# Optimization experiments

Hardware: AMD Instinct MI355X
Metric: run time of the kernel (lower is better)

The kernel has to match this reference:

```python
import jax, jax.numpy as jnp
import numpy as np

B, N_NODES, T_IN = 512, 32, 12
HID, HEADS, OUT_CH, DEG = 64, 8, 9, 8


def setup_inputs() -> dict:
    key = jax.random.key(0)
    ks = jax.random.split(key, 26)
    rn = lambda k, s, sc=0.1: (jax.random.normal(k, s, jnp.float32) * sc)
    E = B * N_NODES * DEG
    src = jax.random.randint(ks[0], (E,), 0, N_NODES, jnp.int32)
    dst = jax.random.randint(ks[1], (E,), 0, N_NODES, jnp.int32)
    off = jnp.repeat(jnp.arange(B, dtype=jnp.int32) * N_NODES, N_NODES * DEG)
    edge_index = jnp.stack([src + off, dst + off])  # block-diagonal batched graph
    x = jax.random.normal(ks[2], (B, N_NODES, T_IN), jnp.float32)
    return {
        "x": x,
        "edge_index": edge_index,
        # gat1: in=T_IN -> HEADS*HID, concat
        "W1": rn(ks[3], (T_IN, HEADS * HID)),
        "a_src1": rn(ks[4], (HEADS, HID)),
        "a_dst1": rn(ks[5], (HEADS, HID)),
        "b1": rn(ks[6], (HEADS * HID,), 0.01),
        # gat2: in=HEADS*HID -> HID, heads=1, mean (concat=False)
        "W2": rn(ks[7], (HEADS * HID, HID), 0.05),
        "a_src2": rn(ks[8], (1, HID)),
        "a_dst2": rn(ks[9], (1, HID)),
        "b2": rn(ks[10], (HID,), 0.01),
        "gamma": jnp.ones((HID,), jnp.float32),
        "beta": jnp.zeros((HID,), jnp.float32),
        # gru1: input_size=N_NODES(=32), hidden=HID
        "Wi1": rn(ks[11], (3 * HID, N_NODES)),
        "Wh1": rn(ks[12], (3 * HID, HID)),
        "bi1": rn(ks[13], (3 * HID,), 0.01),
        "bh1": rn(ks[14], (3 * HID,), 0.01),
        # gru2: input_size=HID, hidden=HID
        "Wi2": rn(ks[15], (3 * HID, HID)),
        "Wh2": rn(ks[16], (3 * HID, HID)),
        "bi2": rn(ks[17], (3 * HID,), 0.01),
        "bh2": rn(ks[18], (3 * HID,), 0.01),
        "Wf": rn(ks[19], (OUT_CH, HID)),
        "bf": rn(ks[20], (OUT_CH,), 0.01),
    }


def _gat_layer(x, src, dst, W, a_s, a_d, b, concat):
    # PyG GATConv (eval mode, self-loops already appended by caller)
    Nn = x.shape[0]
    heads, hc = a_s.shape
    h = (x @ W).reshape(Nn, heads, hc)                 # [N, H, C]
    es = jnp.sum(h * a_s, axis=-1)                     # [N, H]
    ed = jnp.sum(h * a_d, axis=-1)
    e = jax.nn.leaky_relu(es[src] + ed[dst], 0.2)      # [E, H]
    m = jax.ops.segment_max(e, dst, num_segments=Nn)
    p = jnp.exp(e - m[dst])
    s = jax.ops.segment_sum(p, dst, num_segments=Nn)
    alpha = p / (s[dst] + 1e-16)                       # per-dst softmax
    out = jax.ops.segment_sum(h[src] * alpha[:, :, None], dst, num_segments=Nn)
    out = out.reshape(Nn, heads * hc) if concat else out.mean(axis=1)
    return out + b


def _gru(x, Wi, Wh, bi, bh):
    # torch.nn.GRU (batch_first) single layer; x: [B, T, F]
    H = Wh.shape[1]
    xi = x @ Wi.T + bi                                 # [B, T, 3H]
    def step(h, xt):
        gh = h @ Wh.T + bh
        r = jax.nn.sigmoid(xt[:, :H] + gh[:, :H])
        z = jax.nn.sigmoid(xt[:, H:2 * H] + gh[:, H:2 * H])
        n = jnp.tanh(xt[:, 2 * H:] + r * gh[:, 2 * H:])
        hn = (1.0 - z) * n + z * h
        return hn, hn
    h0 = jnp.zeros((x.shape[0], H), x.dtype)
    _, ys = jax.lax.scan(step, h0, jnp.swapaxes(xi, 0, 1))
    return jnp.swapaxes(ys, 0, 1)


def reference(x, edge_index, W1, a_src1, a_dst1, b1, W2, a_src2, a_dst2, b2,
              gamma, beta, Wi1, Wh1, bi1, bh1, Wi2, Wh2, bi2, bh2, Wf, bf):
    Bsz, Nn_, T = x.shape
    Nn = Bsz * Nn_
    xf = x.reshape(Nn, T)                              # dropout is identity in eval
    sl = jnp.arange(Nn, dtype=edge_index.dtype)        # PyG add_self_loops=True
    src = jnp.concatenate([edge_index[0], sl])
    dst = jnp.concatenate([edge_index[1], sl])
    h = jax.nn.elu(_gat_layer(xf, src, dst, W1, a_src1, a_dst1, b1, True))
    h = jax.nn.elu(_gat_layer(h, src, dst, W2, a_src2, a_dst2, b2, False))
    mu = h.mean(-1, keepdims=True)
    var = ((h - mu) ** 2).mean(-1, keepdims=True)
    h = (h - mu) / jnp.sqrt(var + 1e-5) * gamma + beta
    seq = h.reshape(Bsz, Nn_, -1).transpose(0, 2, 1)   # [B, HID(seq), N_NODES(feat)]
    g = _gru(seq, Wi1, Wh1, bi1, bh1)
    g = _gru(g, Wi2, Wh2, bi2, bh2)
    return g[:, -1, :] @ Wf.T + bf                     # [B, OUT_CH]
```

## Files before the change

### kernel.cpp

```cpp
#include <hip/hip_runtime.h>
#include <hip/hip_bf16.h>
#include <stdint.h>

#define BATCH 512
#define NN 32
#define T_IN 12
#define HID 64
#define HEADS 8
#define OUT_CH 9
#define EPB (NN*8)
#define ETOT (EPB+NN)
#define F1 (HEADS*HID)

using u16 = unsigned short;
using u32 = unsigned int;
typedef _Float16 f16;
typedef _Float16 f16x2 __attribute__((ext_vector_type(2)));

__device__ __forceinline__ float bf2f(u16 u){ return __uint_as_float(((u32)u)<<16); }
__device__ __forceinline__ u16 f2bf(float f){
    u32 x = __float_as_uint(f);
    u32 r = (x + 0x7FFFu + ((x>>16)&1u))>>16;
    return (u16)r;
}
__device__ __forceinline__ u32 packf16(float a, float b){
    f16x2 p; p.x=(f16)a; p.y=(f16)b; return __builtin_bit_cast(u32,p);
}
__device__ __forceinline__ u16 f2h16(float a){ f16 h=(f16)a; return __builtin_bit_cast(u16,h); }
__device__ __forceinline__ float lof(u32 w){ return (float)__builtin_bit_cast(f16x2,w).x; }
__device__ __forceinline__ float hif(u32 w){ return (float)__builtin_bit_cast(f16x2,w).y; }
__device__ __forceinline__ float dot2(u32 a, u32 b, float c){
#if __has_builtin(__builtin_amdgcn_fdot2)
    return __builtin_amdgcn_fdot2(__builtin_bit_cast(f16x2,a), __builtin_bit_cast(f16x2,b), c, false);
#else
    return fmaf(lof(a),lof(b), fmaf(hif(a),hif(b), c));
#endif
}
__device__ __forceinline__ float elu1(float x){ return x > 0.f ? x : (__expf(x)-1.f); }
__device__ __forceinline__ float sigm(float x){ return 1.f/(1.f+__expf(-x)); }
__device__ __forceinline__ float tanh_(float x){ return 1.f - 2.f/(__expf(2.f*x)+1.f); }

__global__ __launch_bounds__(256) void k_detect(const u32* __restrict__ xw, int* __restrict__ flag){
    __shared__ int cnt;
    if(threadIdx.x==0) cnt=0;
    __syncthreads();
    int c=0;
    for(int i=threadIdx.x;i<4096;i+=256){
        u32 w=xw[i];
        if(w & 0x7FFFFFFFu){
            u32 el=(w>>7)&0xFFu;
            if(el>=0x90u) c++;
        }
    }
    atomicAdd(&cnt,c);
    __syncthreads();
    if(threadIdx.x==0) *flag = (cnt>256) ? 1 : 0;
}

struct CvtDesc {
    const void* src[20];
    void*       dst[20];
    int         n[20];
};

__global__ __launch_bounds__(256) void k_convert(CvtDesc d, const int* __restrict__ flag){
    const int seg = blockIdx.x;
    const int f = *flag;
    const void* s = d.src[seg];
    const int n = d.n[seg];
    const int stride = gridDim.y*256;
    float* o=(float*)d.dst[seg];
    for(int i=blockIdx.y*256+threadIdx.x;i<n;i+=stride)
        o[i] = f ? ((const float*)s)[i] : bf2f(((const u16*)s)[i]);
}

__global__ __launch_bounds__(256) void k_w2i(const void* __restrict__ W2src, u16* __restrict__ W2i,
                                             const int* __restrict__ flag){
    int i = blockIdx.x*256+threadIdx.x;
    int k=i>>6, j=i&63;
    float v = (*flag)? ((const float*)W2src)[i] : bf2f(((const u16*)W2src)[i]);
    W2i[ (((size_t)(k>>3)*64 + j)<<3) + (k&7) ] = f2h16(v);
}

__global__ __launch_bounds__(256,2) void k_gat1(
    const float* __restrict__ x, const int* __restrict__ ei,
    const float* __restrict__ W1, const float* __restrict__ a_s, const float* __restrict__ a_d,
    const float* __restrict__ b1, u32* __restrict__ h1g)
{
    const int b = blockIdx.x, t = threadIdx.x;
    __shared__ __align__(16) float s_x[NN][12];
    __shared__ float s_W1[T_IN*F1];
    __shared__ __align__(16) u16 s_h[NN][520];
    __shared__ u32 s_aspk[HEADS*32], s_adpk[HEADS*32];
    __shared__ float s_es[NN][HEADS], s_ed[NN][HEADS];
    __shared__ unsigned char s_src[ETOT], s_dst[ETOT];
    __shared__ float s_al[ETOT][HEADS];
    __shared__ int s_cnt[NN], s_off[NN], s_fil[NN];
    __shared__ short s_lst[ETOT];

    for(int i=t;i<NN*T_IN;i+=256) s_x[i/12][i%12] = x[b*NN*T_IN + i];
    for(int i=t;i<T_IN*F1;i+=256) s_W1[i]=W1[i];
    s_aspk[t]=packf16(a_s[2*t],a_s[2*t+1]);
    s_adpk[t]=packf16(a_d[2*t],a_d[2*t+1]);
    if(t<EPB){
        s_src[t] = (unsigned char)(ei[b*EPB+t] - b*NN);
        s_dst[t] = (unsigned char)(ei[(size_t)BATCH*EPB + b*EPB+t] - b*NN);
    }
    if(t<NN){ s_src[EPB+t]=s_dst[EPB+t]=(unsigned char)t; s_cnt[t]=0; s_fil[t]=0; }
    __syncthreads();

    {
        float w0[12], w1[12];
        #pragma unroll
        for(int k=0;k<12;k++){ w0[k]=s_W1[k*F1+t]; w1[k]=s_W1[k*F1+t+256]; }
        for(int n=0;n<NN;n++){
            float xr[12];
            const float4* xp=(const float4*)s_x[n];
            *(float4*)&xr[0]=xp[0]; *(float4*)&xr[4]=xp[1]; *(float4*)&xr[8]=xp[2];
            float A=0.f,B=0.f;
            #pragma unroll
            for(int k=0;k<12;k++){ A=fmaf(xr[k],w0[k],A); B=fmaf(xr[k],w1[k],B); }
            s_h[n][t]=f2h16(A); s_h[n][t+256]=f2h16(B);
        }
    }
    for(int e=t;e<ETOT;e+=256) atomicAdd(&s_cnt[s_dst[e]],1);
    __syncthreads();

    {
        int n=t&31, hd=t>>5;
        const uint4* hp=(const uint4*)((const u16*)s_h[n] + hd*64);
        u32 hw[32];
        #pragma unroll
        for(int q=0;q<8;q++) *(uint4*)&hw[q*4]=hp[q];
        float e1=0.f,e2=0.f;
        #pragma unroll
        for(int k=0;k<32;k++){ e1=dot2(hw[k],s_aspk[hd*32+k],e1); e2=dot2(hw[k],s_adpk[hd*32+k],e2); }
        s_es[n][hd]=e1; s_ed[n][hd]=e2;
    }
    if(t==0){ int o=0; for(int i=0;i<NN;i++){ s_off[i]=o; o+=s_cnt[i]; } }
    __syncthreads();

    for(int e=t;e<ETOT;e+=256){
        int d=s_dst[e]; int p=atomicAdd(&s_fil[d],1); s_lst[s_off[d]+p]=(short)e;
    }
    for(int e=t;e<ETOT;e+=256){
        int s=s_src[e], d=s_dst[e];
        #pragma unroll
        for(int hd=0;hd<HEADS;hd++){
            float v = s_es[s][hd]+s_ed[d][hd];
            s_al[e][hd] = v>0.f? v : 0.2f*v;
        }
    }
    __syncthreads();

    {
        int d=t>>3, hd=t&7;
        int o=s_off[d], c=s_cnt[d];
        float m=-1e30f;
        for(int i=0;i<c;i++) m = fmaxf(m, s_al[s_lst[o+i]][hd]);
        float ss=0.f;
        for(int i=0;i<c;i++){ int e=s_lst[o+i]; float p=__expf(s_al[e][hd]-m); s_al[e][hd]=p; ss+=p; }
        float inv = 1.f/(ss+1e-16f);
        for(int i=0;i<c;i++) s_al[s_lst[o+i]][hd]*=inv;
    }
    __syncthreads();

    {
        int d=t&31, hd=t>>5;
        int o=s_off[d], cnt=s_cnt[d];
        size_t obase = ((size_t)(b*NN+d))*256 + hd*32;
        #pragma unroll
        for(int ch=0;ch<4;ch++){
            float acc[16];
            #pragma unroll
            for(int i=0;i<16;i++) acc[i]=0.f;
            for(int i=0;i<cnt;i++){
                int e=s_lst[o+i]; float a=s_al[e][hd]; int sr=s_src[e];
                const uint4* hp=(const uint4*)((const u16*)s_h[sr] + hd*64 + ch*16);
                u32 pw[8];
                *(uint4*)&pw[0]=hp[0]; *(uint4*)&pw[4]=hp[1];
                #pragma unroll
                for(int q=0;q<8;q++){ acc[2*q]+=a*lof(pw[q]); acc[2*q+1]+=a*hif(pw[q]); }
            }
            u32* op = h1g + obase + ch*8;
            #pragma unroll
            for(int j=0;j<8;j++){
                float v0=elu1(acc[2*j]   + b1[hd*64+ch*16+2*j]);
                float v1=elu1(acc[2*j+1] + b1[hd*64+ch*16+2*j+1]);
                op[j]=packf16(v0,v1);
            }
        }
    }
}

__global__ __launch_bounds__(256,2) void k_gat2ln(
    const u32* __restrict__ h1g, const int* __restrict__ ei,
    const uint4* __restrict__ W2i, const float* __restrict__ a_s2, const float* __restrict__ a_d2,
    const float* __restrict__ b2, const float* __restrict__ gam, const float* __restrict__ bet,
    float* __restrict__ hlng)
{
    const int b=blockIdx.x, t=threadIdx.x;
    __shared__ __align__(16) u32 s_h1[NN*260];
    __shared__ float s_h2[NN][HID];
    __shared__ float s_es[NN], s_ed[NN];
    __shared__ unsigned char s_src[ETOT], s_dst[ETOT];
    __shared__ float s_al[ETOT];
    __shared__ int s_cnt[NN], s_off[NN], s_fil[NN];
    __shared__ short s_lst[ETOT];

    { const u32* g = h1g + (size_t)b*8192;
      for(int w=t; w<8192; w+=256){ int n=w>>8, c=w&255; s_h1[n*260+c]=g[w]; } }
    if(t<EPB){
        s_src[t]=(unsigned char)(ei[b*EPB+t]-b*NN);
        s_dst[t]=(unsigned char)(ei[(size_t)BATCH*EPB+b*EPB+t]-b*NN);
    }
    if(t<NN){ s_src[EPB+t]=s_dst[EPB+t]=(unsigned char)t; s_cnt[t]=0; s_fil[t]=0; }
    __syncthreads();

    for(int e=t;e<ETOT;e+=256) atomicAdd(&s_cnt[s_dst[e]],1);
    {
        int n0=(t>>4)<<1, j0=(t&15)<<2;
        const u32* r0=&s_h1[n0*260];
        const u32* r1=&s_h1[(n0+1)*260];
        float a00=0,a01=0,a02=0,a03=0,a10=0,a11=0,a12=0,a13=0;
        for(int kb=0;kb<64;kb++){
            uint4 A0=*(const uint4*)&r0[kb*4];
            uint4 A1=*(const uint4*)&r1[kb*4];
            const uint4* wp=&W2i[kb*64+j0];
            uint4 w0=wp[0], w1=wp[1], w2=wp[2], w3=wp[3];
            a00=dot2(A0.x,w0.x,a00); a00=dot2(A0.y,w0.y,a00); a00=dot2(A0.z,w0.z,a00); a00=dot2(A0.w,w0.w,a00);
            a01=dot2(A0.x,w1.x,a01); a01=dot2(A0.y,w1.y,a01); a01=dot2(A0.z,w1.z,a01); a01=dot2(A0.w,w1.w,a01);
            a02=dot2(A0.x,w2.x,a02); a02=dot2(A0.y,w2.y,a02); a02=dot2(A0.z,w2.z,a02); a02=dot2(A0.w,w2.w,a02);
            a03=dot2(A0.x,w3.x,a03); a03=dot2(A0.y,w3.y,a03); a03=dot2(A0.z,w3.z,a03); a03=dot2(A0.w,w3.w,a03);
            a10=dot2(A1.x,w0.x,a10); a10=dot2(A1.y,w0.y,a10); a10=dot2(A1.z,w0.z,a10); a10=dot2(A1.w,w0.w,a10);
            a11=dot2(A1.x,w1.x,a11); a11=dot2(A1.y,w1.y,a11); a11=dot2(A1.z,w1.z,a11); a11=dot2(A1.w,w1.w,a11);
            a12=dot2(A1.x,w2.x,a12); a12=dot2(A1.y,w2.y,a12); a12=dot2(A1.z,w2.z,a12); a12=dot2(A1.w,w2.w,a12);
            a13=dot2(A1.x,w3.x,a13); a13=dot2(A1.y,w3.y,a13); a13=dot2(A1.z,w3.z,a13); a13=dot2(A1.w,w3.w,a13);
        }
        s_h2[n0][j0]=a00; s_h2[n0][j0+1]=a01; s_h2[n0][j0+2]=a02; s_h2[n0][j0+3]=a03;
        s_h2[n0+1][j0]=a10; s_h2[n0+1][j0+1]=a11; s_h2[n0+1][j0+2]=a12; s_h2[n0+1][j0+3]=a13;
    }
    __syncthreads();

    {
        int n=t>>3, g=t&7;
        float e1=0,e2=0;
        #pragma unroll
        for(int cc=0; cc<8; cc++){
            float hv = s_h2[n][g*8+cc];
            e1 += hv*a_s2[g*8+cc];
            e2 += hv*a_d2[g*8+cc];
        }
        #pragma unroll
        for(int m=1;m<8;m<<=1){ e1 += __shfl_xor(e1,m,64); e2 += __shfl_xor(e2,m,64); }
        if(g==0){ s_es[n]=e1; s_ed[n]=e2; }
    }
    if(t==0){ int o=0; for(int i=0;i<NN;i++){ s_off[i]=o; o+=s_cnt[i]; } }
    __syncthreads();

    for(int e=t;e<ETOT;e+=256){
        int d=s_dst[e]; int p=atomicAdd(&s_fil[d],1); s_lst[s_off[d]+p]=(short)e;
    }
    for(int e=t;e<ETOT;e+=256){
        float v = s_es[s_src[e]] + s_ed[s_dst[e]];
        s_al[e] = v>0.f? v:0.2f*v;
    }
    __syncthreads();

    if(t<NN){
        int o=s_off[t], c=s_cnt[t];
        float m=-1e30f;
        for(int i=0;i<c;i++) m=fmaxf(m, s_al[s_lst[o+i]]);
        float ss=0;
        for(int i=0;i<c;i++){int e=s_lst[o+i]; float p=__expf(s_al[e]-m); s_al[e]=p; ss+=p;}
        float inv=1.f/(ss+1e-16f);
        for(int i=0;i<c;i++) s_al[s_lst[o+i]]*=inv;
    }
    __syncthreads();

    {
        int n=t>>3, g=t&7;
        float acc[8];
        #pragma unroll
        for(int i=0;i<8;i++) acc[i]=0;
        int o=s_off[n], cnt=s_cnt[n];
        for(int i=0;i<cnt;i++){
            int e=s_lst[o+i]; float a=s_al[e]; int sr=s_src[e];
            const float4* hp=(const float4*)&s_h2[sr][g*8];
            float4 v0=hp[0], v1=hp[1];
            acc[0]+=a*v0.x; acc[1]+=a*v0.y; acc[2]+=a*v0.z; acc[3]+=a*v0.w;
            acc[4]+=a*v1.x; acc[5]+=a*v1.y; acc[6]+=a*v1.z; acc[7]+=a*v1.w;
        }
        float sum=0,sq=0;
        #pragma unroll
        for(int i=0;i<8;i++){
            float v = elu1(acc[i] + b2[g*8+i]);
            acc[i]=v; sum+=v; sq+=v*v;
        }
        #pragma unroll
        for(int m=1;m<8;m<<=1){ sum+=__shfl_xor(sum,m,64); sq+=__shfl_xor(sq,m,64); }
        float mu = sum*(1.f/64.f);
        float var = sq*(1.f/64.f) - mu*mu;
        float rs = rsqrtf(var + 1e-5f);
        float* outp = hlng + (size_t)b*HID*NN;
        #pragma unroll
        for(int i=0;i<8;i++){
            int c=g*8+i;
            float v=(acc[i]-mu)*rs*gam[c] + bet[c];
            outp[c*NN + n] = v;
        }
    }
}

__global__ __launch_bounds__(256,2) void k_gruf(
    const float* __restrict__ hlng,
    const float* __restrict__ Wi1, const float* __restrict__ Wh1,
    const float* __restrict__ bi1, const float* __restrict__ bh1,
    const float* __restrict__ Wi2, const float* __restrict__ Wh2,
    const float* __restrict__ bi2, const float* __restrict__ bh2,
    const float* __restrict__ Wf, const float* __restrict__ bfv,
    void* __restrict__ outp, const int* __restrict__ flag)
{
    const int b=blockIdx.x, t=threadIdx.x;
    const int wave=t>>6, lane=t&63;
    const int layer=wave>>1;
    const int s=wave&1;
    const int u=lane;

    __shared__ __align__(16) u32 s_x1[64*16];
    __shared__ __align__(16) u32 s_y[2][32];
    __shared__ __align__(16) u32 s_h1w[32];
    __shared__ __align__(16) u32 s_h2w[32];
    __shared__ float s_p1[4*64];
    __shared__ float s_p2[4*64];
    __shared__ float s_h2f[64];

    { const float2* g=(const float2*)(hlng + (size_t)b*2048);
      for(int w=t;w<1024;w+=256){ float2 v=g[w]; s_x1[w]=packf16(v.x,v.y); } }
    if(t<32){ s_h1w[t]=0u; s_h2w[t]=0u; }

    u32 wiR[16],wiZ[16],wiN[16],whR[16],whZ[16],whN[16];
    if(layer==0){
        const float2* WiF=(const float2*)Wi1;
        const float2* WhF=(const float2*)Wh1;
        #pragma unroll
        for(int k=0;k<8;k++){
            float2 a=WiF[u*16+s*8+k], c=WiF[(64+u)*16+s*8+k], d=WiF[(128+u)*16+s*8+k];
            wiR[k]=packf16(a.x,a.y); wiZ[k]=packf16(c.x,c.y); wiN[k]=packf16(d.x,d.y);
        }
        #pragma unroll
        for(int k=0;k<16;k++){
            float2 a=WhF[u*32+s*16+k], c=WhF[(64+u)*32+s*16+k], d=WhF[(128+u)*32+s*16+k];
            whR[k]=packf16(a.x,a.y); whZ[k]=packf16(c.x,c.y); whN[k]=packf16(d.x,d.y);
        }
    } else {
        const float2* WiF=(const float2*)Wi2;
        const float2* WhF=(const float2*)Wh2;
        #pragma unroll
        for(int k=0;k<16;k++){
            float2 a=WiF[u*32+s*16+k], c=WiF[(64+u)*32+s*16+k], d=WiF[(128+u)*32+s*16+k];
            wiR[k]=packf16(a.x,a.y); wiZ[k]=packf16(c.x,c.y); wiN[k]=packf16(d.x,d.y);
            float2 e=WhF[u*32+s*16+k], f=WhF[(64+u)*32+s*16+k], g2=WhF[(128+u)*32+s*16+k];
            whR[k]=packf16(e.x,e.y); whZ[k]=packf16(f.x,f.y); whN[k]=packf16(g2.x,g2.y);
        }
    }
    float br=0.f,bz=0.f,bxn=0.f,bhn=0.f,h=0.f;
    if(s==0){
        const float* bi = layer? bi2:bi1;
        const float* bh = layer? bh2:bh1;
        br=bi[u]+bh[u]; bz=bi[64+u]+bh[64+u]; bxn=bi[128+u]; bhn=bh[128+u];
    }
    float* sp = layer? s_p2 : s_p1;
    __syncthreads();

    for(int it=0; it<=64; ++it){
        float pr=0.f,pz=0.f,pxn=0.f,phn=0.f;
        bool act;
        if(layer==0){
            act = (it<64);
            if(act){
                u32 xw[8], hw[16];
                const uint4* xp=(const uint4*)&s_x1[it*16+s*8];
                *(uint4*)&xw[0]=xp[0]; *(uint4*)&xw[4]=xp[1];
                const uint4* hp=(const uint4*)&s_h1w[s*16];
                #pragma unroll
                for(int q=0;q<4;q++) *(uint4*)&hw[q*4]=hp[q];
                #pragma unroll
                for(int k=0;k<8;k++){ pr=dot2(xw[k],wiR[k],pr); pz=dot2(xw[k],wiZ[k],pz); pxn=dot2(xw[k],wiN[k],pxn); }
                #pragma unroll
                for(int k=0;k<16;k++){ pr=dot2(hw[k],whR[k],pr); pz=dot2(hw[k],whZ[k],pz); phn=dot2(hw[k],whN[k],phn); }
            }
        } else {
            act = (it>=1);
            if(act){
                u32 xw[16], hw[16];
                const uint4* xp=(const uint4*)&s_y[(it-1)&1][s*16];
                #pragma unroll
                for(int q=0;q<4;q++) *(uint4*)&xw[q*4]=xp[q];
                const uint4* hp=(const uint4*)&s_h2w[s*16];
                #pragma unroll
                for(int q=0;q<4;q++) *(uint4*)&hw[q*4]=hp[q];
                #pragma unroll
                for(int k=0;k<16;k++){
                    pr=dot2(xw[k],wiR[k],pr); pz=dot2(xw[k],wiZ[k],pz); pxn=dot2(xw[k],wiN[k],pxn);
                    pr=dot2(hw[k],whR[k],pr); pz=dot2(hw[k],whZ[k],pz); phn=dot2(hw[k],whN[k],phn);
                }
            }
        }
        if(act && s==1){ sp[u]=pr; sp[64+u]=pz; sp[128+u]=pxn; sp[192+u]=phn; }
        __syncthreads();
        if(act && s==0){
            float ar = pr + sp[u] + br;
            float az = pz + sp[64+u] + bz;
            float axn = pxn + sp[128+u] + bxn;
            float ahn = phn + sp[192+u] + bhn;
            float r=sigm(ar), z=sigm(az);
            float n=tanh_(axn + r*ahn);
            h=(1.f-z)*n + z*h;
            u16 hp16=f2h16(h);
            if(layer==0){
                ((u16*)s_h1w)[u]=hp16;
                ((u16*)s_y[it&1])[u]=hp16;
            } else {
                ((u16*)s_h2w)[u]=hp16;
                if(it==64) s_h2f[u]=h;
            }
        }
        __syncthreads();
    }

    if(t<OUT_CH){
        float acc=bfv[t];
        #pragma unroll
        for(int i=0;i<64;i++) acc += s_h2f[i]*Wf[t*64+i];
        if(*flag) ((float*)outp)[b*OUT_CH+t]=acc;
        else      ((u16*)outp)[b*OUT_CH+t]=f2bf(acc);
    }
}

extern "C" void kernel_launch(void* const* d_in, const int* in_sizes, int n_in,
                              void* d_out, int out_size, void* d_ws, size_t ws_size,
                              hipStream_t stream)
{
    char* ws=(char*)d_ws;
    int* flag = (int*)ws;
    float* cf = (float*)(ws + 256);
    float* c_x   = cf; cf+=196608;
    float* c_W1  = cf; cf+=6144;
    float* c_as1 = cf; cf+=512;
    float* c_ad1 = cf; cf+=512;
    float* c_b1  = cf; cf+=512;
    float* c_as2 = cf; cf+=64;
    float* c_ad2 = cf; cf+=64;
    float* c_b2  = cf; cf+=64;
    float* c_gam = cf; cf+=64;
    float* c_bet = cf; cf+=64;
    float* c_Wi1 = cf; cf+=6144;
    float* c_Wh1 = cf; cf+=12288;
    float* c_bi1 = cf; cf+=192;
    float* c_bh1 = cf; cf+=192;
    float* c_Wi2 = cf; cf+=12288;
    float* c_Wh2 = cf; cf+=12288;
    float* c_bi2 = cf; cf+=192;
    float* c_bh2 = cf; cf+=192;
    float* c_Wf  = cf; cf+=576;
    float* c_bf  = cf; cf+=9;
    uintptr_t p = ((uintptr_t)cf + 255) & ~(uintptr_t)255;
    u16* c_W2i = (u16*)p;
    p = (p + 32768*2 + 255) & ~(uintptr_t)255;
    u32* h1g = (u32*)p;
    p = (p + (size_t)BATCH*NN*256*4 + 255) & ~(uintptr_t)255;
    float* hlng = (float*)p;

    const int* ei = (const int*)d_in[1];

    CvtDesc d;
    const int srcIdx[20] = {0,2,3,4,5,7,8,9,10,11,12,13,14,15,16,17,18,19,20,21};
    void* dsts[20] = {c_x,c_W1,c_as1,c_ad1,c_b1,c_as2,c_ad2,c_b2,c_gam,c_bet,
                      c_Wi1,c_Wh1,c_bi1,c_bh1,c_Wi2,c_Wh2,c_bi2,c_bh2,c_Wf,c_bf};
    const int ns[20] = {196608,6144,512,512,512,64,64,64,64,64,
                        6144,12288,192,192,12288,12288,192,192,576,9};
    for(int i=0;i<20;i++){ d.src[i]=d_in[srcIdx[i]]; d.dst[i]=dsts[i]; d.n[i]=ns[i]; }

    k_detect <<<dim3(1),dim3(256),0,stream>>>((const u32*)d_in[0], flag);
    k_convert<<<dim3(20,8),dim3(256),0,stream>>>(d, flag);
    k_w2i    <<<dim3(128),dim3(256),0,stream>>>(d_in[6], c_W2i, flag);
    k_gat1   <<<dim3(BATCH),dim3(256),0,stream>>>(c_x,ei,c_W1,c_as1,c_ad1,c_b1,h1g);
    k_gat2ln <<<dim3(BATCH),dim3(256),0,stream>>>(h1g,ei,(const uint4*)c_W2i,c_as2,c_ad2,c_b2,c_gam,c_bet,hlng);
    k_gruf   <<<dim3(BATCH),dim3(256),0,stream>>>(hlng,c_Wi1,c_Wh1,c_bi1,c_bh1,
                                                  c_Wi2,c_Wh2,c_bi2,c_bh2,c_Wf,c_bf,d_out,flag);
}
```

Before: 262.6 us.

## Parallelize GAT softmax with shared atomics and use wave shuffles in GRU

The per-destination serial softmax loops in both GAT kernels are replaced by edge-parallel passes. These use shared-memory atomicMax on order-preserving encoded floats and atomicAdd for the sums, and normalization is folded into the aggregation epilogue. The GAT1 aggregation now processes 32 channels per pass instead of 16. The GRU kernel splits each hidden unit's dot product across the two half-waves and combines them with a lane shuffle, with double-buffered hidden state. This removes one __syncthreads and the shared-memory partial exchange per timestep, at the cost of atomic contention, more accumulator registers, and a change in floating-point summation order.

```diff
diff --git a/kernel.cpp b/kernel.cpp
--- a/kernel.cpp
+++ b/kernel.cpp
@@ -39,6 +39,13 @@
 __device__ __forceinline__ float elu1(float x){ return x > 0.f ? x : (__expf(x)-1.f); }
 __device__ __forceinline__ float sigm(float x){ return 1.f/(1.f+__expf(-x)); }
 __device__ __forceinline__ float tanh_(float x){ return 1.f - 2.f/(__expf(2.f*x)+1.f); }
+__device__ __forceinline__ u32 fenc(float v){
+    u32 b=__float_as_uint(v);
+    return (b&0x80000000u) ? ~b : (b|0x80000000u);
+}
+__device__ __forceinline__ float fdec(u32 k){
+    return __uint_as_float((k&0x80000000u) ? (k&0x7FFFFFFFu) : ~k);
+}
 
 __global__ __launch_bounds__(256) void k_detect(const u32* __restrict__ xw, int* __restrict__ flag){
     __shared__ int cnt;
@@ -95,6 +102,8 @@
     __shared__ float s_es[NN][HEADS], s_ed[NN][HEADS];
     __shared__ unsigned char s_src[ETOT], s_dst[ETOT];
     __shared__ float s_al[ETOT][HEADS];
+    __shared__ u32 s_mx[NN*HEADS];
+    __shared__ float s_sm[NN*HEADS], s_inv[NN*HEADS];
     __shared__ int s_cnt[NN], s_off[NN], s_fil[NN];
     __shared__ short s_lst[ETOT];
 
@@ -102,6 +111,7 @@
     for(int i=t;i<T_IN*F1;i+=256) s_W1[i]=W1[i];
     s_aspk[t]=packf16(a_s[2*t],a_s[2*t+1]);
     s_adpk[t]=packf16(a_d[2*t],a_d[2*t+1]);
+    s_mx[t]=0u; s_sm[t]=0.f;
     if(t<EPB){
         s_src[t] = (unsigned char)(ei[b*EPB+t] - b*NN);
         s_dst[t] = (unsigned char)(ei[(size_t)BATCH*EPB + b*EPB+t] - b*NN);
@@ -143,50 +153,51 @@
     for(int e=t;e<ETOT;e+=256){
         int d=s_dst[e]; int p=atomicAdd(&s_fil[d],1); s_lst[s_off[d]+p]=(short)e;
     }
-    for(int e=t;e<ETOT;e+=256){
-        int s=s_src[e], d=s_dst[e];
-        #pragma unroll
-        for(int hd=0;hd<HEADS;hd++){
-            float v = s_es[s][hd]+s_ed[d][hd];
-            s_al[e][hd] = v>0.f? v : 0.2f*v;
-        }
-    }
-    __syncthreads();
-
-    {
-        int d=t>>3, hd=t&7;
-        int o=s_off[d], c=s_cnt[d];
-        float m=-1e30f;
-        for(int i=0;i<c;i++) m = fmaxf(m, s_al[s_lst[o+i]][hd]);
-        float ss=0.f;
-        for(int i=0;i<c;i++){ int e=s_lst[o+i]; float p=__expf(s_al[e][hd]-m); s_al[e][hd]=p; ss+=p; }
-        float inv = 1.f/(ss+1e-16f);
-        for(int i=0;i<c;i++) s_al[s_lst[o+i]][hd]*=inv;
-    }
+    for(int i=t;i<ETOT*HEADS;i+=256){
+        int e=i>>3, hd=i&7;
+        int sr=s_src[e], d=s_dst[e];
+        float v = s_es[sr][hd]+s_ed[d][hd];
+        v = v>0.f? v : 0.2f*v;
+        s_al[e][hd]=v;
+        atomicMax(&s_mx[d*8+hd], fenc(v));
+    }
+    __syncthreads();
+
+    for(int i=t;i<ETOT*HEADS;i+=256){
+        int e=i>>3, hd=i&7;
+        int d=s_dst[e];
+        float p=__expf(s_al[e][hd]-fdec(s_mx[d*8+hd]));
+        s_al[e][hd]=p;
+        atomicAdd(&s_sm[d*8+hd], p);
+    }
+    __syncthreads();
+    s_inv[t]=1.f/(s_sm[t]+1e-16f);
     __syncthreads();
 
     {
         int d=t&31, hd=t>>5;
         int o=s_off[d], cnt=s_cnt[d];
+        float inv=s_inv[d*8+hd];
         size_t obase = ((size_t)(b*NN+d))*256 + hd*32;
         #pragma unroll
-        for(int ch=0;ch<4;ch++){
-            float acc[16];
+        for(int ch=0;ch<2;ch++){
+            float acc[32];
             #pragma unroll
-            for(int i=0;i<16;i++) acc[i]=0.f;
+            for(int i=0;i<32;i++) acc[i]=0.f;
             for(int i=0;i<cnt;i++){
                 int e=s_lst[o+i]; float a=s_al[e][hd]; int sr=s_src[e];
-                const uint4* hp=(const uint4*)((const u16*)s_h[sr] + hd*64 + ch*16);
-                u32 pw[8];
+                const uint4* hp=(const uint4*)((const u16*)s_h[sr] + hd*64 + ch*32);
+                u32 pw[16];
                 *(uint4*)&pw[0]=hp[0]; *(uint4*)&pw[4]=hp[1];
-                #pragma unroll
-                for(int q=0;q<8;q++){ acc[2*q]+=a*lof(pw[q]); acc[2*q+1]+=a*hif(pw[q]); }
+                *(uint4*)&pw[8]=hp[2]; *(uint4*)&pw[12]=hp[3];
+                #pragma unroll
+                for(int q=0;q<16;q++){ acc[2*q]+=a*lof(pw[q]); acc[2*q+1]+=a*hif(pw[q]); }
             }
-            u32* op = h1g + obase + ch*8;
+            u32* op = h1g + obase + ch*16;
             #pragma unroll
-            for(int j=0;j<8;j++){
-                float v0=elu1(acc[2*j]   + b1[hd*64+ch*16+2*j]);
-                float v1=elu1(acc[2*j+1] + b1[hd*64+ch*16+2*j+1]);
+            for(int j=0;j<16;j++){
+                float v0=elu1(acc[2*j]*inv   + b1[hd*64+ch*32+2*j]);
+                float v1=elu1(acc[2*j+1]*inv + b1[hd*64+ch*32+2*j+1]);
                 op[j]=packf16(v0,v1);
             }
         }
@@ -205,6 +216,8 @@
     __shared__ float s_es[NN], s_ed[NN];
     __shared__ unsigned char s_src[ETOT], s_dst[ETOT];
     __shared__ float s_al[ETOT];
+    __shared__ u32 s_mx[NN];
+    __shared__ float s_sm[NN], s_inv[NN];
     __shared__ int s_cnt[NN], s_off[NN], s_fil[NN];
     __shared__ short s_lst[ETOT];
 
@@ -214,7 +227,8 @@
         s_src[t]=(unsigned char)(ei[b*EPB+t]-b*NN);
         s_dst[t]=(unsigned char)(ei[(size_t)BATCH*EPB+b*EPB+t]-b*NN);
     }
-    if(t<NN){ s_src[EPB+t]=s_dst[EPB+t]=(unsigned char)t; s_cnt[t]=0; s_fil[t]=0; }
+    if(t<NN){ s_src[EPB+t]=s_dst[EPB+t]=(unsigned char)t;
+              s_cnt[t]=0; s_fil[t]=0; s_mx[t]=0u; s_sm[t]=0.f; }
     __syncthreads();
 
     for(int e=t;e<ETOT;e+=256) atomicAdd(&s_cnt[s_dst[e]],1);
@@ -262,20 +276,22 @@
         int d=s_dst[e]; int p=atomicAdd(&s_fil[d],1); s_lst[s_off[d]+p]=(short)e;
     }
     for(int e=t;e<ETOT;e+=256){
-        float v = s_es[s_src[e]] + s_ed[s_dst[e]];
-        s_al[e] = v>0.f? v:0.2f*v;
-    }
-    __syncthreads();
-
-    if(t<NN){
-        int o=s_off[t], c=s_cnt[t];
-        float m=-1e30f;
-        for(int i=0;i<c;i++) m=fmaxf(m, s_al[s_lst[o+i]]);
-        float ss=0;
-        for(int i=0;i<c;i++){int e=s_lst[o+i]; float p=__expf(s_al[e]-m); s_al[e]=p; ss+=p;}
-        float inv=1.f/(ss+1e-16f);
-        for(int i=0;i<c;i++) s_al[s_lst[o+i]]*=inv;
-    }
+        int d=s_dst[e];
+        float v = s_es[s_src[e]] + s_ed[d];
+        v = v>0.f? v:0.2f*v;
+        s_al[e]=v;
+        atomicMax(&s_mx[d], fenc(v));
+    }
+    __syncthreads();
+
+    for(int e=t;e<ETOT;e+=256){
+        int d=s_dst[e];
+        float p=__expf(s_al[e]-fdec(s_mx[d]));
+        s_al[e]=p;
+        atomicAdd(&s_sm[d], p);
+    }
+    __syncthreads();
+    if(t<NN) s_inv[t]=1.f/(s_sm[t]+1e-16f);
     __syncthreads();
 
     {
@@ -284,6 +300,7 @@
         #pragma unroll
         for(int i=0;i<8;i++) acc[i]=0;
         int o=s_off[n], cnt=s_cnt[n];
+        float inv=s_inv[n];
         for(int i=0;i<cnt;i++){
             int e=s_lst[o+i]; float a=s_al[e]; int sr=s_src[e];
             const float4* hp=(const float4*)&s_h2[sr][g*8];
@@ -294,7 +311,7 @@
         float sum=0,sq=0;
         #pragma unroll
         for(int i=0;i<8;i++){
-            float v = elu1(acc[i] + b2[g*8+i]);
+            float v = elu1(acc[i]*inv + b2[g*8+i]);
             acc[i]=v; sum+=v; sq+=v*v;
         }
         #pragma unroll
@@ -324,20 +341,18 @@
     const int b=blockIdx.x, t=threadIdx.x;
     const int wave=t>>6, lane=t&63;
     const int layer=wave>>1;
-    const int s=wave&1;
-    const int u=lane;
+    const int ublk=wave&1;
+    const int uu=lane&31, s=lane>>5;
+    const int u=ublk*32+uu;
 
     __shared__ __align__(16) u32 s_x1[64*16];
-    __shared__ __align__(16) u32 s_y[2][32];
-    __shared__ __align__(16) u32 s_h1w[32];
-    __shared__ __align__(16) u32 s_h2w[32];
-    __shared__ float s_p1[4*64];
-    __shared__ float s_p2[4*64];
+    __shared__ __align__(16) u32 s_h1[2][32];
+    __shared__ __align__(16) u32 s_h2[2][32];
     __shared__ float s_h2f[64];
 
     { const float2* g=(const float2*)(hlng + (size_t)b*2048);
       for(int w=t;w<1024;w+=256){ float2 v=g[w]; s_x1[w]=packf16(v.x,v.y); } }
-    if(t<32){ s_h1w[t]=0u; s_h2w[t]=0u; }
+    if(t<32){ s_h1[0][t]=0u; s_h1[1][t]=0u; s_h2[0][t]=0u; s_h2[1][t]=0u; }
 
     u32 wiR[16],wiZ[16],wiN[16],whR[16],whZ[16],whN[16];
     if(layer==0){
@@ -364,25 +379,23 @@
             whR[k]=packf16(e.x,e.y); whZ[k]=packf16(f.x,f.y); whN[k]=packf16(g2.x,g2.y);
         }
     }
-    float br=0.f,bz=0.f,bxn=0.f,bhn=0.f,h=0.f;
-    if(s==0){
-        const float* bi = layer? bi2:bi1;
-        const float* bh = layer? bh2:bh1;
-        br=bi[u]+bh[u]; bz=bi[64+u]+bh[64+u]; bxn=bi[128+u]; bhn=bh[128+u];
-    }
-    float* sp = layer? s_p2 : s_p1;
+    const float* bi = layer? bi2:bi1;
+    const float* bh = layer? bh2:bh1;
+    float br=bi[u]+bh[u], bz=bi[64+u]+bh[64+u], bxn=bi[128+u], bhn=bh[128+u];
+    float h=0.f;
     __syncthreads();
 
     for(int it=0; it<=64; ++it){
+        const int pb=(it-1)&1, cb=it&1;
         float pr=0.f,pz=0.f,pxn=0.f,phn=0.f;
         bool act;
         if(layer==0){
-            act = (it<64);
+            act=(it<64);
             if(act){
                 u32 xw[8], hw[16];
                 const uint4* xp=(const uint4*)&s_x1[it*16+s*8];
                 *(uint4*)&xw[0]=xp[0]; *(uint4*)&xw[4]=xp[1];
-                const uint4* hp=(const uint4*)&s_h1w[s*16];
+                const uint4* hp=(const uint4*)&s_h1[pb][s*16];
                 #pragma unroll
                 for(int q=0;q<4;q++) *(uint4*)&hw[q*4]=hp[q];
                 #pragma unroll
@@ -391,13 +404,13 @@
                 for(int k=0;k<16;k++){ pr=dot2(hw[k],whR[k],pr); pz=dot2(hw[k],whZ[k],pz); phn=dot2(hw[k],whN[k],phn); }
             }
         } else {
-            act = (it>=1);
+            act=(it>=1);
             if(act){
                 u32 xw[16], hw[16];
-                const uint4* xp=(const uint4*)&s_y[(it-1)&1][s*16];
+                const uint4* xp=(const uint4*)&s_h1[pb][s*16];
                 #pragma unroll
                 for(int q=0;q<4;q++) *(uint4*)&xw[q*4]=xp[q];
-                const uint4* hp=(const uint4*)&s_h2w[s*16];
+                const uint4* hp=(const uint4*)&s_h2[pb][s*16];
                 #pragma unroll
                 for(int q=0;q<4;q++) *(uint4*)&hw[q*4]=hp[q];
                 #pragma unroll
@@ -407,23 +420,18 @@
                 }
             }
         }
-        if(act && s==1){ sp[u]=pr; sp[64+u]=pz; sp[128+u]=pxn; sp[192+u]=phn; }
-        __syncthreads();
-        if(act && s==0){
-            float ar = pr + sp[u] + br;
-            float az = pz + sp[64+u] + bz;
-            float axn = pxn + sp[128+u] + bxn;
-            float ahn = phn + sp[192+u] + bhn;
-            float r=sigm(ar), z=sigm(az);
-            float n=tanh_(axn + r*ahn);
+        if(act){
+            pr  += __shfl_xor(pr ,32,64);
+            pz  += __shfl_xor(pz ,32,64);
+            pxn += __shfl_xor(pxn,32,64);
+            phn += __shfl_xor(phn,32,64);
+            float r=sigm(pr+br), z=sigm(pz+bz);
+            float n=tanh_(pxn+bxn + r*(phn+bhn));
             h=(1.f-z)*n + z*h;
-            u16 hp16=f2h16(h);
-            if(layer==0){
-                ((u16*)s_h1w)[u]=hp16;
-                ((u16*)s_y[it&1])[u]=hp16;
-            } else {
-                ((u16*)s_h2w)[u]=hp16;
-                if(it==64) s_h2f[u]=h;
+            if(s==0){
+                u16 hv=f2h16(h);
+                if(layer==0) ((u16*)s_h1[cb])[u]=hv;
+                else { ((u16*)s_h2[cb])[u]=hv; if(it==64) s_h2f[u]=h; }
             }
         }
         __syncthreads();
```

Measured after the change: 260.0 us. About the same (-1.0%).
